# Optimization experiments

Measured on AMD Instinct MI355X. Metric: run time of the kernel, lower is better.

## Reference

```python
import jax, jax.numpy as jnp
import numpy as np

N = 50000
E = 800000
IN_CH = 128
HID = 64
H1 = 4  # heads in gat1
NEG_SLOPE = 0.2


def _gat_layer(x, src, dst, W, a_src, a_dst, bias, heads, ch):
    # x: [N, F_in]; W: [F_in, heads*ch]; a_src/a_dst: [heads, ch]; bias: [heads*ch]
    n = x.shape[0]
    h = (x @ W).reshape(n, heads, ch)                       # [N, H, C]
    alpha_src = jnp.einsum('nhc,hc->nh', h, a_src)          # [N, H]
    alpha_dst = jnp.einsum('nhc,hc->nh', h, a_dst)          # [N, H]
    e = jax.nn.leaky_relu(alpha_src[src] + alpha_dst[dst], NEG_SLOPE)  # [E, H]
    # segment softmax over incoming edges of each destination node
    m = jax.ops.segment_max(e, dst, num_segments=n)         # [N, H]
    ex = jnp.exp(e - m[dst])                                # [E, H]
    denom = jax.ops.segment_sum(ex, dst, num_segments=n)    # [N, H]
    alpha = ex / (denom[dst] + 1e-16)                       # [E, H]
    out = jax.ops.segment_sum(alpha[:, :, None] * h[src], dst, num_segments=n)  # [N, H, C]
    return out.reshape(n, heads * ch) + bias


def setup_inputs() -> dict:
    key = jax.random.key(0)
    ks = jax.random.split(key, 12)
    x = jax.random.normal(ks[0], (N, IN_CH), dtype=jnp.float32)
    edge_index = jax.random.randint(ks[1], (2, E), 0, N, dtype=jnp.int64)
    s1 = 1.0 / np.sqrt(IN_CH)
    s2 = 1.0 / np.sqrt(H1 * HID)
    s3 = 1.0 / np.sqrt(HID)
    return {
        'x': x,
        'edge_index': edge_index,
        'W1': jax.random.uniform(ks[2], (IN_CH, H1 * HID), jnp.float32, -s1, s1),
        'att_src1': jax.random.uniform(ks[3], (H1, HID), jnp.float32, -s1, s1),
        'att_dst1': jax.random.uniform(ks[4], (H1, HID), jnp.float32, -s1, s1),
        'b1': jnp.zeros((H1 * HID,), jnp.float32),
        'W2': jax.random.uniform(ks[5], (H1 * HID, HID), jnp.float32, -s2, s2),
        'att_src2': jax.random.uniform(ks[6], (1, HID), jnp.float32, -s2, s2),
        'att_dst2': jax.random.uniform(ks[7], (1, HID), jnp.float32, -s2, s2),
        'b2': jnp.zeros((HID,), jnp.float32),
        'W_out': jax.random.uniform(ks[8], (HID, 1), jnp.float32, -s3, s3),
        'b_out': jnp.zeros((1,), jnp.float32),
    }


def reference(x, edge_index, W1, att_src1, att_dst1, b1, W2, att_src2, att_dst2, b2, W_out, b_out):
    # add self-loops (PyG GATConv default)
    loops = jnp.arange(N, dtype=edge_index.dtype)
    src = jnp.concatenate([edge_index[0], loops])
    dst = jnp.concatenate([edge_index[1], loops])
    h = jax.nn.relu(_gat_layer(x, src, dst, W1, att_src1, att_dst1, b1, H1, HID))
    h = jax.nn.relu(_gat_layer(h, src, dst, W2, att_src2, att_dst2, b2, 1, HID))
    return (h @ W_out + b_out).squeeze(-1)  # [N]
```

## Files before the change

### kernel.cpp

```cpp
#include <hip/hip_runtime.h>
#include <hip/hip_bf16.h>
#include <math.h>

#define N_NODES 50000
#define N_EDGES 800000
#define EE_TOTAL (N_EDGES + N_NODES)
#define CAP 64

#define GEMM1_BLOCKS ((N_NODES + 63) / 64)
#define SCAT_BLOCKS ((EE_TOTAL + 1023) / 1024)
#define FUSED_BLOCKS (GEMM1_BLOCKS + SCAT_BLOCKS)
#define AGG1_BLOCKS 25000

typedef __attribute__((ext_vector_type(8))) short bf16x8;
typedef __attribute__((ext_vector_type(4))) float f32x4;

__device__ __forceinline__ float bf2f(unsigned short s) {
  return __uint_as_float((unsigned)s << 16);
}
__device__ __forceinline__ unsigned short f2bf(float f) {
  unsigned u = __float_as_uint(f);
  return (unsigned short)((u + 0x7FFFu + ((u >> 16) & 1u)) >> 16);
}
__device__ __forceinline__ float lrelu(float e) { return e > 0.f ? e : 0.2f * e; }

__global__ void prep_kernel(const float* __restrict__ W1, const float* __restrict__ W2,
                            unsigned short* __restrict__ W1t, unsigned short* __restrict__ W2t,
                            int* __restrict__ counts) {
  int i = blockIdx.x * blockDim.x + threadIdx.x;
  if (i < N_NODES) counts[i] = 0;
  if (i < 256 * 128) W1t[i] = f2bf(W1[(i & 127) * 256 + (i >> 7)]);
  if (i < 64 * 256) W2t[i] = f2bf(W2[(i & 255) * 64 + (i >> 8)]);
}

__device__ __forceinline__ void scatter_body(int sid, int t,
                                             const int* __restrict__ src,
                                             const int* __restrict__ dst,
                                             int* __restrict__ counts,
                                             unsigned short* __restrict__ col) {
  int base = sid * 1024 + t * 4;
  int ss[4], dd[4];
#pragma unroll
  for (int k = 0; k < 4; ++k) {
    int i = base + k;
    if (i < N_EDGES) { ss[k] = src[i]; dd[k] = dst[i]; }
    else if (i < EE_TOTAL) { ss[k] = i - N_EDGES; dd[k] = ss[k]; }
    else { ss[k] = 0; dd[k] = -1; }
  }
#pragma unroll
  for (int k = 0; k < 4; ++k) {
    if (dd[k] >= 0) {
      int pos = atomicAdd(&counts[dd[k]], 1);
      if (pos < CAP) col[(size_t)dd[k] * CAP + pos] = (unsigned short)ss[k];
    }
  }
}

__global__ __launch_bounds__(256) void fused_kernel(const int* __restrict__ src,
                                                    const int* __restrict__ dst,
                                                    int* __restrict__ counts,
                                                    unsigned short* __restrict__ col,
                                                    const float* __restrict__ A,
                                                    const unsigned short* __restrict__ Bt,
                                                    unsigned short* __restrict__ Cb,
                                                    const float* __restrict__ att_s,
                                                    const float* __restrict__ att_d,
                                                    float* __restrict__ as_out,
                                                    float* __restrict__ ad_out) {
  __shared__ unsigned short Bs[256 * 128];
  int b = blockIdx.x;
  int t = threadIdx.x;
  bool is_gemm;
  int id;
  if (b < 2 * GEMM1_BLOCKS) { is_gemm = (b & 1) == 0; id = b >> 1; }
  else { is_gemm = false; id = b - GEMM1_BLOCKS; }

  if (!is_gemm) {
    scatter_body(id, t, src, dst, counts, col);
    return;
  }

  const int M = N_NODES;
  int lane = t & 63, w = t >> 6;
  int row0 = id * 64;
#pragma unroll
  for (int i = 0; i < 16; ++i) {
    int idx = i * 256 + t;
    int n = idx >> 4;
    uint4 v = ((const uint4*)Bt)[idx];
    int byte = (idx * 16) ^ ((n & 7) << 4);
    *(uint4*)((char*)Bs + byte) = v;
  }
  __syncthreads();
  int rl = lane & 15, kg = lane >> 4;
  f32x4 acc[4][4] = {};
  for (int ks = 0; ks < 4; ++ks) {
    bf16x8 af[4], bfr[4];
#pragma unroll
    for (int rb = 0; rb < 4; ++rb) {
      int row = row0 + rb * 16 + rl;
      float4 v0 = make_float4(0.f, 0.f, 0.f, 0.f), v1 = v0;
      if (row < M) {
        const float* p = A + (size_t)row * 128 + ks * 32 + kg * 8;
        v0 = *(const float4*)p;
        v1 = *(const float4*)(p + 4);
      }
      bf16x8 a;
      a[0] = (short)f2bf(v0.x); a[1] = (short)f2bf(v0.y);
      a[2] = (short)f2bf(v0.z); a[3] = (short)f2bf(v0.w);
      a[4] = (short)f2bf(v1.x); a[5] = (short)f2bf(v1.y);
      a[6] = (short)f2bf(v1.z); a[7] = (short)f2bf(v1.w);
      af[rb] = a;
    }
#pragma unroll
    for (int cb = 0; cb < 4; ++cb) {
      int n = w * 64 + cb * 16 + rl;
      int byte = (n * 256 + ks * 64 + kg * 16) ^ ((n & 7) << 4);
      bfr[cb] = *(const bf16x8*)((char*)Bs + byte);
    }
#pragma unroll
    for (int rb = 0; rb < 4; ++rb)
#pragma unroll
      for (int cb = 0; cb < 4; ++cb)
        acc[rb][cb] = __builtin_amdgcn_mfma_f32_16x16x32_bf16(af[rb], bfr[cb], acc[rb][cb], 0, 0, 0);
  }
  float asv[4], adv[4];
#pragma unroll
  for (int cb = 0; cb < 4; ++cb) {
    int c = w * 64 + cb * 16 + rl;
    asv[cb] = att_s[c];
    adv[cb] = att_d[c];
  }
#pragma unroll
  for (int rb = 0; rb < 4; ++rb) {
#pragma unroll
    for (int r = 0; r < 4; ++r) {
      int row = row0 + rb * 16 + kg * 4 + r;
      bool ok = row < M;
      float sp = 0.f, dp = 0.f;
#pragma unroll
      for (int cb = 0; cb < 4; ++cb) {
        float v = acc[rb][cb][r];
        if (ok) Cb[(size_t)row * 256 + w * 64 + cb * 16 + rl] = f2bf(v);
        sp += v * asv[cb];
        dp += v * adv[cb];
      }
#pragma unroll
      for (int off = 1; off < 16; off <<= 1) {
        sp += __shfl_xor(sp, off, 64);
        dp += __shfl_xor(dp, off, 64);
      }
      if (ok && rl == 0) {
        as_out[row * 4 + w] = sp;
        ad_out[row * 4 + w] = dp;
      }
    }
  }
}

__global__ __launch_bounds__(256) void gemm2_kernel(const unsigned short* __restrict__ A,
                                                    const unsigned short* __restrict__ Bt,
                                                    unsigned short* __restrict__ Cb,
                                                    const float* __restrict__ att_s,
                                                    const float* __restrict__ att_d,
                                                    float* __restrict__ as_out,
                                                    float* __restrict__ ad_out) {
  __shared__ unsigned short Bs[64 * 256];
  const int M = N_NODES;
  int t = threadIdx.x;
  int lane = t & 63, w = t >> 6;
  int row0 = blockIdx.x * 64;
#pragma unroll
  for (int i = 0; i < 8; ++i) {
    int idx = i * 256 + t;
    int n = idx >> 5;
    uint4 v = ((const uint4*)Bt)[idx];
    int byte = (idx * 16) ^ ((n & 7) << 4);
    *(uint4*)((char*)Bs + byte) = v;
  }
  __syncthreads();
  int rl = lane & 15, kg = lane >> 4;
  int arow = row0 + w * 16 + rl;
  f32x4 acc[4] = {};
  for (int ks = 0; ks < 8; ++ks) {
    bf16x8 a = {};
    if (arow < M) a = *(const bf16x8*)(A + (size_t)arow * 256 + ks * 32 + kg * 8);
#pragma unroll
    for (int cb = 0; cb < 4; ++cb) {
      int n = cb * 16 + rl;
      int byte = (n * 512 + ks * 64 + kg * 16) ^ ((n & 7) << 4);
      bf16x8 bfrag = *(const bf16x8*)((char*)Bs + byte);
      acc[cb] = __builtin_amdgcn_mfma_f32_16x16x32_bf16(a, bfrag, acc[cb], 0, 0, 0);
    }
  }
  float asv[4], adv[4];
#pragma unroll
  for (int cb = 0; cb < 4; ++cb) {
    int c = cb * 16 + rl;
    asv[cb] = att_s[c];
    adv[cb] = att_d[c];
  }
#pragma unroll
  for (int r = 0; r < 4; ++r) {
    int orow = row0 + w * 16 + kg * 4 + r;
    bool ok = orow < M;
    float sp = 0.f, dp = 0.f;
#pragma unroll
    for (int cb = 0; cb < 4; ++cb) {
      float v = acc[cb][r];
      if (ok) Cb[(size_t)orow * 64 + cb * 16 + rl] = f2bf(v);
      sp += v * asv[cb];
      dp += v * adv[cb];
    }
#pragma unroll
    for (int off = 1; off < 16; off <<= 1) {
      sp += __shfl_xor(sp, off, 64);
      dp += __shfl_xor(dp, off, 64);
    }
    if (ok && rl == 0) {
      as_out[orow] = sp;
      ad_out[orow] = dp;
    }
  }
}

__global__ __launch_bounds__(256) void agg1_kernel(const unsigned short* __restrict__ h1b,
                                                   const float* __restrict__ as,
                                                   const float* __restrict__ ad,
                                                   const int* __restrict__ counts,
                                                   const unsigned short* __restrict__ col,
                                                   const float* __restrict__ b1,
                                                   unsigned short* __restrict__ x2b) {
  __shared__ int s_lds[8][64];
  __shared__ float p_lds[8][64];
  int bid = blockIdx.x;
  int head = (bid & 7) >> 1;
  int idx = (bid >> 3) * 2 + (bid & 1);
  int t = threadIdx.x;
  int hw = t >> 5;
  int sl = t & 31;
  int node = idx * 8 + hw;
  int cnt = min(counts[node], CAP);
  const unsigned short* cbase = col + (size_t)node * CAP;
  float adn = ad[node * 4 + head];
  float den = 0.f;
#pragma unroll
  for (int c0 = 0; c0 < 64; c0 += 32) {
    int e = c0 + sl;
    int s = node;
    float p = 0.f;
    if (e < cnt) {
      s = cbase[e];
      p = __expf(lrelu(as[s * 4 + head] + adn));
    }
    s_lds[hw][e] = s;
    p_lds[hw][e] = p;
    den += p;
  }
#pragma unroll
  for (int off = 1; off < 32; off <<= 1) den += __shfl_xor(den, off, 64);
  int e_off = sl >> 3, cl = sl & 7;
  const unsigned short* hb = h1b + head * 64 + cl * 8;
  float acc[8] = {};
  int nq = (cnt + 7) & ~7;
  for (int j = 0; j < nq; j += 8) {
    int ea = j + e_off, eb = j + 4 + e_off;
    int sa = s_lds[hw][ea], sb = s_lds[hw][eb];
    float pa = p_lds[hw][ea], pb = p_lds[hw][eb];
    bf16x8 va = *(const bf16x8*)(hb + (size_t)sa * 256);
    bf16x8 vb = *(const bf16x8*)(hb + (size_t)sb * 256);
#pragma unroll
    for (int k = 0; k < 8; ++k) {
      acc[k] += pa * bf2f((unsigned short)va[k]) + pb * bf2f((unsigned short)vb[k]);
    }
  }
#pragma unroll
  for (int k = 0; k < 8; ++k) {
    acc[k] += __shfl_xor(acc[k], 8, 64);
    acc[k] += __shfl_xor(acc[k], 16, 64);
  }
  if (e_off == 0) {
    float inv = 1.f / (den + 1e-16f);
    int ch = head * 64 + cl * 8;
    float4 blo = *(const float4*)(b1 + ch);
    float4 bhi = *(const float4*)(b1 + ch + 4);
    float bb[8] = {blo.x, blo.y, blo.z, blo.w, bhi.x, bhi.y, bhi.z, bhi.w};
    bf16x8 o;
#pragma unroll
    for (int k = 0; k < 8; ++k) o[k] = (short)f2bf(fmaxf(acc[k] * inv + bb[k], 0.f));
    *(bf16x8*)(x2b + (size_t)node * 256 + ch) = o;
  }
}

__global__ __launch_bounds__(256) void agg2_final_kernel(const unsigned short* __restrict__ h2b,
                                                         const float* __restrict__ as,
                                                         const float* __restrict__ ad,
                                                         const int* __restrict__ counts,
                                                         const unsigned short* __restrict__ col,
                                                         const float* __restrict__ b2,
                                                         const float* __restrict__ Wout,
                                                         const float* __restrict__ bout,
                                                         float* __restrict__ out) {
  __shared__ int s_lds[4][64];
  __shared__ float p_lds[4][64];
  int t = threadIdx.x;
  int lane = t & 63, w = t >> 6;
  int node = blockIdx.x * 4 + w;
  if (node >= N_NODES) return;
  int cnt = min(counts[node], CAP);
  const unsigned short* cbase = col + (size_t)node * CAP;
  float adn = ad[node];
  int g = lane >> 4, sl = lane & 15;
  int s = node;
  float p = 0.f;
  if (lane < cnt) {
    s = cbase[lane];
    p = __expf(lrelu(as[s] + adn));
  }
  s_lds[w][lane] = s;
  p_lds[w][lane] = p;
  float den = p;
#pragma unroll
  for (int off = 1; off < 64; off <<= 1) den += __shfl_xor(den, off, 64);
  float acc[4] = {};
  int nq = (cnt + 7) & ~7;
  for (int j = 0; j < nq; j += 8) {
    int e0 = j + g, e1 = j + 4 + g;
    int s0 = s_lds[w][e0], s1 = s_lds[w][e1];
    float p0 = p_lds[w][e0], p1 = p_lds[w][e1];
    ushort4 v0 = *(const ushort4*)(h2b + (size_t)s0 * 64 + sl * 4);
    ushort4 v1 = *(const ushort4*)(h2b + (size_t)s1 * 64 + sl * 4);
    acc[0] += p0 * bf2f(v0.x) + p1 * bf2f(v1.x);
    acc[1] += p0 * bf2f(v0.y) + p1 * bf2f(v1.y);
    acc[2] += p0 * bf2f(v0.z) + p1 * bf2f(v1.z);
    acc[3] += p0 * bf2f(v0.w) + p1 * bf2f(v1.w);
  }
#pragma unroll
  for (int k = 0; k < 4; ++k) {
    acc[k] += __shfl_xor(acc[k], 16, 64);
    acc[k] += __shfl_xor(acc[k], 32, 64);
  }
  float inv = 1.f / (den + 1e-16f);
  int ch = sl * 4;
  float4 b4 = *(const float4*)(b2 + ch);
  float4 w4 = *(const float4*)(Wout + ch);
  float part = fmaxf(acc[0] * inv + b4.x, 0.f) * w4.x +
               fmaxf(acc[1] * inv + b4.y, 0.f) * w4.y +
               fmaxf(acc[2] * inv + b4.z, 0.f) * w4.z +
               fmaxf(acc[3] * inv + b4.w, 0.f) * w4.w;
#pragma unroll
  for (int off = 1; off < 16; off <<= 1) part += __shfl_xor(part, off, 64);
  if (lane == 0) out[node] = part + bout[0];
}

extern "C" void kernel_launch(void* const* d_in, const int* in_sizes, int n_in,
                              void* d_out, int out_size, void* d_ws, size_t ws_size,
                              hipStream_t stream) {
  const float* x    = (const float*)d_in[0];
  const int*   ei   = (const int*)d_in[1];
  const float* W1   = (const float*)d_in[2];
  const float* as1w = (const float*)d_in[3];
  const float* ad1w = (const float*)d_in[4];
  const float* b1   = (const float*)d_in[5];
  const float* W2   = (const float*)d_in[6];
  const float* as2w = (const float*)d_in[7];
  const float* ad2w = (const float*)d_in[8];
  const float* b2   = (const float*)d_in[9];
  const float* Wout = (const float*)d_in[10];
  const float* bout = (const float*)d_in[11];
  float* out = (float*)d_out;

  const int* src = ei;
  const int* dst = ei + N_EDGES;

  char* ws = (char*)d_ws;
  size_t off = 0;
  auto alloc = [&](size_t bytes) -> char* {
    char* p = ws + off;
    off += (bytes + 255) & ~(size_t)255;
    return p;
  };
  int*            counts = (int*)alloc((size_t)N_NODES * 4);
  unsigned short* col    = (unsigned short*)alloc((size_t)N_NODES * CAP * 2);
  unsigned short* W1t    = (unsigned short*)alloc((size_t)256 * 128 * 2);
  unsigned short* W2t    = (unsigned short*)alloc((size_t)64 * 256 * 2);
  unsigned short* x2b    = (unsigned short*)alloc((size_t)N_NODES * 256 * 2);
  unsigned short* hbuf   = (unsigned short*)alloc((size_t)N_NODES * 256 * 2);
  float*          as1    = (float*)alloc((size_t)N_NODES * 4 * 4);
  float*          ad1    = (float*)alloc((size_t)N_NODES * 4 * 4);
  float*          as2    = (float*)alloc((size_t)N_NODES * 4);
  float*          ad2    = (float*)alloc((size_t)N_NODES * 4);

  unsigned short* h1b = hbuf;
  unsigned short* h2b = hbuf;

  const int node_blocks4 = (N_NODES + 3) / 4;
  const int gemm_blocks = (N_NODES + 63) / 64;

  prep_kernel<<<(N_NODES + 255) / 256, 256, 0, stream>>>(W1, W2, W1t, W2t, counts);

  fused_kernel<<<FUSED_BLOCKS, 256, 0, stream>>>(src, dst, counts, col,
                                                 x, W1t, h1b, as1w, ad1w, as1, ad1);

  agg1_kernel<<<AGG1_BLOCKS, 256, 0, stream>>>(h1b, as1, ad1, counts, col, b1, x2b);

  gemm2_kernel<<<gemm_blocks, 256, 0, stream>>>(x2b, W2t, h2b, as2w, ad2w, as2, ad2);
  agg2_final_kernel<<<node_blocks4, 256, 0, stream>>>(h2b, as2, ad2, counts, col, b2,
                                                      Wout, bout, out);
}
```

Before: 153.9 us.

## Transpose layer-1 attention scalars to head-major and software-pipeline agg1 gathers

The GEMM1 epilogue now writes the source/destination attention logits in head-major [4][N] layout, and agg1 reads them from per-head rows. agg1 also skips the second 32-edge score chunk when the node has 32 or fewer edges. Its gather loop now steps 4 edges at a time and prefetches the next neighbor row while accumulating the current one, where it previously loaded 8 edges per iteration. The aim is tighter score-gather locality, less wasted work on low-degree nodes, and less padding, though each iteration now has fewer loads in flight.

Measured after the change: 151.5 us. No clear change (-1.6%).

```diff
diff --git a/kernel.cpp b/kernel.cpp
--- a/kernel.cpp
+++ b/kernel.cpp
@@ -151,8 +151,8 @@
         dp += __shfl_xor(dp, off, 64);
       }
       if (ok && rl == 0) {
-        as_out[row * 4 + w] = sp;
-        ad_out[row * 4 + w] = dp;
+        as_out[w * M + row] = sp;
+        ad_out[w * M + row] = dp;
       }
     }
   }
@@ -225,14 +225,15 @@
 }
 
 __global__ __launch_bounds__(256) void agg1_kernel(const unsigned short* __restrict__ h1b,
-                                                   const float* __restrict__ as,
-                                                   const float* __restrict__ ad,
+                                                   const float* __restrict__ as_t,
+                                                   const float* __restrict__ ad_t,
                                                    const int* __restrict__ counts,
                                                    const unsigned short* __restrict__ col,
                                                    const float* __restrict__ b1,
                                                    unsigned short* __restrict__ x2b) {
   __shared__ int s_lds[8][64];
   __shared__ float p_lds[8][64];
+  const int M = N_NODES;
   int bid = blockIdx.x;
   int head = (bid & 7) >> 1;
   int idx = (bid >> 3) * 2 + (bid & 1);
@@ -242,16 +243,28 @@
   int node = idx * 8 + hw;
   int cnt = min(counts[node], CAP);
   const unsigned short* cbase = col + (size_t)node * CAP;
-  float adn = ad[node * 4 + head];
+  const float* as_h = as_t + (size_t)head * M;
+  float adn = ad_t[(size_t)head * M + node];
   float den = 0.f;
-#pragma unroll
-  for (int c0 = 0; c0 < 64; c0 += 32) {
-    int e = c0 + sl;
+  {
+    int e = sl;
     int s = node;
     float p = 0.f;
     if (e < cnt) {
       s = cbase[e];
-      p = __expf(lrelu(as[s * 4 + head] + adn));
+      p = __expf(lrelu(as_h[s] + adn));
+    }
+    s_lds[hw][e] = s;
+    p_lds[hw][e] = p;
+    den += p;
+  }
+  if (cnt > 32) {
+    int e = 32 + sl;
+    int s = node;
+    float p = 0.f;
+    if (e < cnt) {
+      s = cbase[e];
+      p = __expf(lrelu(as_h[s] + adn));
     }
     s_lds[hw][e] = s;
     p_lds[hw][e] = p;
@@ -262,18 +275,20 @@
   int e_off = sl >> 3, cl = sl & 7;
   const unsigned short* hb = h1b + head * 64 + cl * 8;
   float acc[8] = {};
-  int nq = (cnt + 7) & ~7;
-  for (int j = 0; j < nq; j += 8) {
-    int ea = j + e_off, eb = j + 4 + e_off;
-    int sa = s_lds[hw][ea], sb = s_lds[hw][eb];
-    float pa = p_lds[hw][ea], pb = p_lds[hw][eb];
-    bf16x8 va = *(const bf16x8*)(hb + (size_t)sa * 256);
+  int nq = (cnt + 3) & ~3;
+  int sa = s_lds[hw][e_off];
+  float pa = p_lds[hw][e_off];
+  bf16x8 va = *(const bf16x8*)(hb + (size_t)sa * 256);
+  for (int j = 4; j < nq; j += 4) {
+    int sb = s_lds[hw][j + e_off];
+    float pb = p_lds[hw][j + e_off];
     bf16x8 vb = *(const bf16x8*)(hb + (size_t)sb * 256);
 #pragma unroll
-    for (int k = 0; k < 8; ++k) {
-      acc[k] += pa * bf2f((unsigned short)va[k]) + pb * bf2f((unsigned short)vb[k]);
-    }
-  }
+    for (int k = 0; k < 8; ++k) acc[k] += pa * bf2f((unsigned short)va[k]);
+    va = vb; pa = pb;
+  }
+#pragma unroll
+  for (int k = 0; k < 8; ++k) acc[k] += pa * bf2f((unsigned short)va[k]);
 #pragma unroll
   for (int k = 0; k < 8; ++k) {
     acc[k] += __shfl_xor(acc[k], 8, 64);
```
